# Kernel optimization log

Hardware: AMD Instinct MI355X
Metric: run time of the kernel (lower is better)

The kernel has to match this reference:

```python
import jax, jax.numpy as jnp
import numpy as np

KERNEL_SIZE = 5

def setup_inputs() -> dict:
    key = jax.random.key(0)
    k1, k2, k3 = jax.random.split(key, 3)
    H = W = 4096
    stdv = 1.0 / KERNEL_SIZE
    return {
        "input": jax.random.normal(k1, (H, W), dtype=jnp.float32),
        "K_hit": jax.random.uniform(k2, (KERNEL_SIZE, KERNEL_SIZE), dtype=jnp.float32, minval=-stdv, maxval=stdv),
        "K_miss": jax.random.uniform(k3, (KERNEL_SIZE, KERNEL_SIZE), dtype=jnp.float32, minval=-stdv, maxval=stdv),
    }

def _hitmiss(x, K_hit, K_miss):
    k = K_hit.shape[0]
    c = (k - 1) // 2
    Hout = x.shape[0] - 2 * c
    Wout = x.shape[1] - 2 * c
    # Fmap[i,j] = min_{di,dj}(x[i+di, j+dj] - K_hit[di,dj]) - max_{di,dj}(x[i+di, j+dj] - K_miss[di,dj])
    mn = jnp.full((Hout, Wout), jnp.inf, dtype=x.dtype)
    mx = jnp.full((Hout, Wout), -jnp.inf, dtype=x.dtype)
    for di in range(k):          # small fixed k*k loop over structuring-element offsets
        for dj in range(k):
            w = x[di:di + Hout, dj:dj + Wout]
            mn = jnp.minimum(mn, w - K_hit[di, dj])
            mx = jnp.maximum(mx, w - K_miss[di, dj])
    return mn - mx

def reference(input, K_hit, K_miss):
    return _hitmiss(input, K_hit, K_miss)
```

## Files before the change

### kernel.cpp

```cpp
#include <hip/hip_runtime.h>
#include <math.h>


constexpr int KS = 5;
constexpr int HH = 4096;
constexpr int WW = 4096;
constexpr int HO = HH - (KS - 1);
constexpr int WO = WW - (KS - 1);

__global__ __launch_bounds__(256) void hitmiss_kernel(
    const float* __restrict__ x,
    const float* __restrict__ kh,
    const float* __restrict__ km,
    float* __restrict__ out)
{
    const int g   = blockIdx.x * blockDim.x + threadIdx.x;
    const int row = blockIdx.y;
    const int j0  = g * 4;
    if (j0 >= WO) return;

    float khr[KS * KS], kmr[KS * KS];
#pragma unroll
    for (int i = 0; i < KS * KS; ++i) {
        khr[i] = kh[i];
        kmr[i] = km[i];
    }

    float mn[4], mx[4];
#pragma unroll
    for (int p = 0; p < 4; ++p) {
        mn[p] = INFINITY;
        mx[p] = -INFINITY;
    }

#pragma unroll
    for (int di = 0; di < KS; ++di) {
        const float* rp = x + (size_t)(row + di) * WW + j0;
        float4 a = *reinterpret_cast<const float4*>(rp);
        float4 b = *reinterpret_cast<const float4*>(rp + 4);
        float v[8] = {a.x, a.y, a.z, a.w, b.x, b.y, b.z, b.w};
#pragma unroll
        for (int dj = 0; dj < KS; ++dj) {
            const float h = khr[di * KS + dj];
            const float m = kmr[di * KS + dj];
#pragma unroll
            for (int p = 0; p < 4; ++p) {
                mn[p] = fminf(mn[p], v[dj + p] - h);
                mx[p] = fmaxf(mx[p], v[dj + p] - m);
            }
        }
    }

    float4 o;
    o.x = mn[0] - mx[0];
    o.y = mn[1] - mx[1];
    o.z = mn[2] - mx[2];
    o.w = mn[3] - mx[3];
    *reinterpret_cast<float4*>(out + (size_t)row * WO + j0) = o;
}

extern "C" void kernel_launch(void* const* d_in, const int* in_sizes, int n_in,
                              void* d_out, int out_size, void* d_ws, size_t ws_size,
                              hipStream_t stream) {
    const float* x  = (const float*)d_in[0];
    const float* kh = (const float*)d_in[1];
    const float* km = (const float*)d_in[2];
    float* out = (float*)d_out;

    dim3 block(256, 1, 1);
    dim3 grid((WO / 4 + 255) / 256, HO, 1);
    hipLaunchKernelGGL(hitmiss_kernel, grid, block, 0, stream, x, kh, km, out);
}
```

Measured before the change: 133.6 us.

## Compute four output rows per thread reusing loaded input rows in registers

Each thread now produces a 4x4 output block instead of 1x4. It loads 8 input rows once into registers and reuses them across the four overlapping 5-row windows, cutting global/L2 load traffic per output from 5 rows to 2 rows. The cost is higher register pressure from the 8x8 value array and the weight arrays, and a quarter as many blocks in the grid. HO=4092 is divisible by 4, so coverage stays exact.

```diff
diff --git a/kernel.cpp b/kernel.cpp
--- a/kernel.cpp
+++ b/kernel.cpp
@@ -7,6 +7,7 @@
 constexpr int WW = 4096;
 constexpr int HO = HH - (KS - 1);
 constexpr int WO = WW - (KS - 1);
+constexpr int CG = WO / 4;
 
 __global__ __launch_bounds__(256) void hitmiss_kernel(
     const float* __restrict__ x,
@@ -14,49 +15,69 @@
     const float* __restrict__ km,
     float* __restrict__ out)
 {
-    const int g   = blockIdx.x * blockDim.x + threadIdx.x;
-    const int row = blockIdx.y;
-    const int j0  = g * 4;
-    if (j0 >= WO) return;
+    const int cg = blockIdx.x * blockDim.x + threadIdx.x;
+    if (cg >= CG) return;
+    const int j0 = cg * 4;
+    const int r0 = blockIdx.y * 4;
 
-    float khr[KS * KS], kmr[KS * KS];
+    float wh[KS * KS], wm[KS * KS];
 #pragma unroll
     for (int i = 0; i < KS * KS; ++i) {
-        khr[i] = kh[i];
-        kmr[i] = km[i];
+        wh[i] = kh[i];
+        wm[i] = km[i];
     }
 
-    float mn[4], mx[4];
+    float v[8][8];
+
 #pragma unroll
-    for (int p = 0; p < 4; ++p) {
-        mn[p] = INFINITY;
-        mx[p] = -INFINITY;
+    for (int r = 0; r < 5; ++r) {
+        const float* rp = x + (size_t)(r0 + r) * WW + j0;
+        float4 a = *reinterpret_cast<const float4*>(rp);
+        float4 b = *reinterpret_cast<const float4*>(rp + 4);
+        v[r][0] = a.x; v[r][1] = a.y; v[r][2] = a.z; v[r][3] = a.w;
+        v[r][4] = b.x; v[r][5] = b.y; v[r][6] = b.z; v[r][7] = b.w;
     }
 
 #pragma unroll
-    for (int di = 0; di < KS; ++di) {
-        const float* rp = x + (size_t)(row + di) * WW + j0;
-        float4 a = *reinterpret_cast<const float4*>(rp);
-        float4 b = *reinterpret_cast<const float4*>(rp + 4);
-        float v[8] = {a.x, a.y, a.z, a.w, b.x, b.y, b.z, b.w};
+    for (int orow = 0; orow < 4; ++orow) {
+        if (orow < 3) {
+            const int r = orow + 5;
+            const float* rp = x + (size_t)(r0 + r) * WW + j0;
+            float4 a = *reinterpret_cast<const float4*>(rp);
+            float4 b = *reinterpret_cast<const float4*>(rp + 4);
+            v[r][0] = a.x; v[r][1] = a.y; v[r][2] = a.z; v[r][3] = a.w;
+            v[r][4] = b.x; v[r][5] = b.y; v[r][6] = b.z; v[r][7] = b.w;
+        }
+
+        float mn[4], mx[4];
 #pragma unroll
-        for (int dj = 0; dj < KS; ++dj) {
-            const float h = khr[di * KS + dj];
-            const float m = kmr[di * KS + dj];
+        for (int p = 0; p < 4; ++p) {
+            mn[p] = INFINITY;
+            mx[p] = -INFINITY;
+        }
+
 #pragma unroll
-            for (int p = 0; p < 4; ++p) {
-                mn[p] = fminf(mn[p], v[dj + p] - h);
-                mx[p] = fmaxf(mx[p], v[dj + p] - m);
+        for (int di = 0; di < KS; ++di) {
+            const float* row = v[orow + di];
+#pragma unroll
+            for (int dj = 0; dj < KS; ++dj) {
+                const float h = wh[di * KS + dj];
+                const float m = wm[di * KS + dj];
+#pragma unroll
+                for (int p = 0; p < 4; ++p) {
+                    mn[p] = fminf(mn[p], row[dj + p] - h);
+                    mx[p] = fmaxf(mx[p], row[dj + p] - m);
+                }
             }
         }
+
+        float4 o;
+        o.x = mn[0] - mx[0];
+        o.y = mn[1] - mx[1];
+        o.z = mn[2] - mx[2];
+        o.w = mn[3] - mx[3];
+        *reinterpret_cast<float4*>(out + (size_t)(r0 + orow) * WO + j0) = o;
     }
-
-    float4 o;
-    o.x = mn[0] - mx[0];
-    o.y = mn[1] - mx[1];
-    o.z = mn[2] - mx[2];
-    o.w = mn[3] - mx[3];
-    *reinterpret_cast<float4*>(out + (size_t)row * WO + j0) = o;
 }
 
 extern "C" void kernel_launch(void* const* d_in, const int* in_sizes, int n_in,
@@ -68,6 +89,6 @@
     float* out = (float*)d_out;
 
     dim3 block(256, 1, 1);
-    dim3 grid((WO / 4 + 255) / 256, HO, 1);
+    dim3 grid((CG + 255) / 256, HO / 4, 1);
     hipLaunchKernelGGL(hitmiss_kernel, grid, block, 0, stream, x, kh, km, out);
 }
```

Measured after the change: 124.8 us. 6.6% less time.
